# Optimization experiments

Hardware: AMD Instinct MI355X
Metric: run time of the kernel (lower is better)

The kernel has to match this reference:

```python
import jax, jax.numpy as jnp
import numpy as np

N_HEAD = 16
TEMPERATURE = 1.0
LORA_SCALING = 16.0 / 8.0  # lora_alpha / r


def setup_inputs() -> dict:
    key = jax.random.key(0)
    B, S, D, E, R = 4, 1024, 1024, 8, 8
    ks = jax.random.split(key, 24)
    it = iter(ks)

    def nrm(shape, s):
        return (jax.random.normal(next(it), shape, jnp.float32) * s)

    inp = {}
    inp['x'] = jax.random.normal(next(it), (B, S, D), jnp.float32)
    inp['conv_w'] = nrm((D, D, 3), 0.02)
    inp['conv_b'] = jnp.zeros((D,), jnp.float32)
    inp['pool_w'] = nrm((1, D), 0.02)
    inp['pool_b'] = jnp.zeros((1,), jnp.float32)
    inp['rlin_w'] = nrm((E, D), 0.02)
    inp['rlin_b'] = jnp.zeros((E,), jnp.float32)
    for p, has_bias in (('q', True), ('k', False), ('v', True), ('o', True)):
        inp[p + 'W'] = nrm((D, D), 0.02)
        if has_bias:
            inp[p + 'b'] = jnp.zeros((D,), jnp.float32)
        inp[p + 'A'] = nrm((E, R, D), 0.02)
        inp[p + 'B'] = nrm((E, D, R), 0.02)
    return inp


def _router(x, conv_w, conv_b, pool_w, pool_b, rlin_w, rlin_b):
    # Conv1d(kernel=3, padding=1) over sequence, channels = n_state
    xc = jax.lax.conv_general_dilated(
        x.transpose(0, 2, 1), conv_w, (1,), [(1, 1)],
        dimension_numbers=('NCH', 'OIH', 'NCH')) + conv_b[None, :, None]
    xp = xc.transpose(0, 2, 1)                      # [B, S, D]
    scores = xp @ pool_w.T + pool_b                 # [B, S, 1]
    w = jax.nn.softmax(scores, axis=1)
    pooled = jnp.sum(w * xp, axis=1)                # [B, D]
    logits = pooled @ rlin_w.T + rlin_b             # [B, E]
    return jax.nn.softmax(logits / TEMPERATURE, axis=-1)


def _moe_linear(x, W, b, A, Bm, route):
    base = x @ W.T
    if b is not None:
        base = base + b
    h = jnp.einsum('bsd,erd->besr', x, A)           # [B, E, S, r]
    lora = jnp.einsum('besr,enr,be->bsn', h, Bm, route)
    return base + LORA_SCALING * lora


def reference(x, conv_w, conv_b, pool_w, pool_b, rlin_w, rlin_b,
              qW, qb, qA, qB, kW, kA, kB, vW, vb, vA, vB, oW, ob, oA, oB):
    B, S, D = x.shape
    H = N_HEAD
    dh = D // H
    route = _router(x, conv_w, conv_b, pool_w, pool_b, rlin_w, rlin_b)

    q = _moe_linear(x, qW, qb, qA, qB, route)
    k = _moe_linear(x, kW, None, kA, kB, route)
    v = _moe_linear(x, vW, vb, vA, vB, route)

    scale = dh ** (-0.25)
    qh = q.reshape(B, S, H, dh).transpose(0, 2, 1, 3) * scale   # [B,H,S,dh]
    kh = k.reshape(B, S, H, dh).transpose(0, 2, 3, 1) * scale   # [B,H,dh,S]
    vh = v.reshape(B, S, H, dh).transpose(0, 2, 1, 3)           # [B,H,S,dh]

    qk = (qh @ kh).astype(jnp.float32)                          # [B,H,S,S]
    w = jax.nn.softmax(qk, axis=-1).astype(q.dtype)
    wv = (w @ vh).transpose(0, 2, 1, 3).reshape(B, S, D)

    out = _moe_linear(wv, oW, ob, oA, oB, route)
    return out, qk
```

## Files before the change

### kernel.cpp

```cpp
#include <hip/hip_runtime.h>
#include <cstdint>

typedef unsigned short u16;
typedef __bf16 bf16_t;
typedef bf16_t bf16x8 __attribute__((ext_vector_type(8)));
typedef float f32x4 __attribute__((ext_vector_type(4)));

#define B_ 4
#define S_ 1024
#define D_ 1024
#define E_ 8
#define R_ 8
#define H_ 16
#define DH_ 64

#define GLOAD16(gp, lp) __builtin_amdgcn_global_load_lds( \
        (const __attribute__((address_space(1))) void*)(gp), \
        (__attribute__((address_space(3))) void*)(lp), 16, 0, 0)

static __device__ __forceinline__ u16 f2b(float f){
    union { float f; uint32_t i; } v; v.f = f;
    uint32_t i = v.i;
    uint32_t r = i + 0x7FFFu + ((i >> 16) & 1u);
    return (u16)(r >> 16);
}

__global__ void k_pre(const float4* x, const float* qB, const float* kB,
                      const float* vB, const float* oB,
                      const float* conv_w, const float* conv_b,
                      const float* pool_w, const float* pool_b,
                      ushort4* x16, ushort4* B16v, float* cwp_part, float* constk){
    const int NCVT = 2048;
    const int NX = B_*S_*D_/4;
    const int NB = E_*D_*R_/4;
    if (blockIdx.x < NCVT){
        const int NTOT = NX + 4*NB;
        for (int i = blockIdx.x*blockDim.x + threadIdx.x; i < NTOT; i += NCVT*blockDim.x){
            if (i < NX){
                float4 v = x[i];
                ushort4 o; o.x=f2b(v.x); o.y=f2b(v.y); o.z=f2b(v.z); o.w=f2b(v.w);
                x16[i] = o;
            } else {
                int j = i - NX;
                int p = j >> 14, e = j & (NB-1);
                const float4* src = (p==0)?(const float4*)qB:(p==1)?(const float4*)kB
                                  :(p==2)?(const float4*)vB:(const float4*)oB;
                float4 v = src[e];
                ushort4 o; o.x=f2b(v.x); o.y=f2b(v.y); o.z=f2b(v.z); o.w=f2b(v.w);
                B16v[p*NB + e] = o;
            }
        }
    } else {
        int idx = blockIdx.x - NCVT;
        if (idx < 96){
            int bid = idx % 12, ob = idx / 12;
            int j = bid*256 + threadIdx.x;
            int t = j >> 10, i = j & 1023;
            float acc = 0.f;
            for (int o = ob*128; o < ob*128 + 128; ++o)
                acc += pool_w[o] * conv_w[(size_t)o*3072 + i*3 + t];
            cwp_part[ob*3072 + j] = acc;
        } else {
            __shared__ float red[256];
            float acc = 0.f;
            for (int o = threadIdx.x; o < D_; o += 256) acc += pool_w[o] * conv_b[o];
            red[threadIdx.x] = acc; __syncthreads();
            for (int s = 128; s > 0; s >>= 1){
                if (threadIdx.x < s) red[threadIdx.x] += red[threadIdx.x+s];
                __syncthreads();
            }
            if (threadIdx.x == 0) *constk = red[0] + pool_b[0];
        }
    }
}

__global__ void k_h(const float* x, const float* cwp_part, float* h){
    __shared__ float cw[3072];
    int b = blockIdx.y;
    for (int j = threadIdx.x; j < 3072; j += 256){
        float s = 0.f;
        for (int ob = 0; ob < 8; ++ob) s += cwp_part[ob*3072 + j];
        cw[j] = s;
    }
    __syncthreads();
    int w = threadIdx.x >> 6, lane = threadIdx.x & 63;
    int s = blockIdx.x*4 + w;
    const float4* xr = (const float4*)(x + ((size_t)b*S_ + s)*D_);
    const float4* c0 = (const float4*)(cw);
    const float4* c1 = (const float4*)(cw + D_);
    const float4* c2 = (const float4*)(cw + 2*D_);
    float a0 = 0.f, a1 = 0.f, a2 = 0.f;
    #pragma unroll
    for (int it = 0; it < 4; ++it){
        float4 v  = xr[it*64 + lane];
        float4 w0 = c0[it*64 + lane];
        float4 w1 = c1[it*64 + lane];
        float4 w2 = c2[it*64 + lane];
        a0 += v.x*w0.x + v.y*w0.y + v.z*w0.z + v.w*w0.w;
        a1 += v.x*w1.x + v.y*w1.y + v.z*w1.z + v.w*w1.w;
        a2 += v.x*w2.x + v.y*w2.y + v.z*w2.z + v.w*w2.w;
    }
    for (int off = 32; off; off >>= 1){
        a0 += __shfl_down(a0, off);
        a1 += __shfl_down(a1, off);
        a2 += __shfl_down(a2, off);
    }
    if (lane == 0){
        h[(0*B_ + b)*S_ + s] = a0;
        h[(1*B_ + b)*S_ + s] = a1;
        h[(2*B_ + b)*S_ + s] = a2;
    }
}

__global__ void k_xw(const float* x, const float* h, const float* constk, float* xwl){
    int b = blockIdx.y;
    int lane = threadIdx.x & 63;
    int w = threadIdx.x >> 6;
    int i = blockIdx.x*64 + lane;
    __shared__ float red[256];
    __shared__ float wsm_l[S_];
    __shared__ float red3[3][4][64];
    const float* h0 = h + (0*B_ + b)*S_;
    const float* h1 = h + (1*B_ + b)*S_;
    const float* h2 = h + (2*B_ + b)*S_;
    float ck = *constk;
    float mx = -1e30f;
    for (int s = threadIdx.x; s < S_; s += 256){
        float v = h1[s] + ck;
        if (s >= 1)   v += h0[s-1];
        if (s+1 < S_) v += h2[s+1];
        wsm_l[s] = v;
        mx = fmaxf(mx, v);
    }
    red[threadIdx.x] = mx; __syncthreads();
    for (int st = 128; st > 0; st >>= 1){
        if (threadIdx.x < st) red[threadIdx.x] = fmaxf(red[threadIdx.x], red[threadIdx.x+st]);
        __syncthreads();
    }
    mx = red[0]; __syncthreads();
    float sum = 0.f;
    for (int s = threadIdx.x; s < S_; s += 256) sum += __expf(wsm_l[s] - mx);
    red[threadIdx.x] = sum; __syncthreads();
    for (int st = 128; st > 0; st >>= 1){
        if (threadIdx.x < st) red[threadIdx.x] += red[threadIdx.x+st];
        __syncthreads();
    }
    float inv = 1.f / red[0];
    __syncthreads();
    for (int s = threadIdx.x; s < S_; s += 256)
        wsm_l[s] = __expf(wsm_l[s] - mx) * inv;
    __syncthreads();
    const float* xb = x + (size_t)b*S_*D_;
    float a0 = 0.f, a1 = 0.f, a2 = 0.f;
    #pragma unroll 4
    for (int r = w*256; r < (w+1)*256; ++r){
        float xv = xb[(size_t)r*D_ + i];
        float w1 = wsm_l[r];
        float w0 = (r+1 < S_) ? wsm_l[r+1] : 0.f;
        float w2 = (r >= 1)   ? wsm_l[r-1] : 0.f;
        a0 += w0*xv; a1 += w1*xv; a2 += w2*xv;
    }
    red3[0][w][lane] = a0; red3[1][w][lane] = a1; red3[2][w][lane] = a2;
    __syncthreads();
    if (w == 0){
        a0 = red3[0][0][lane] + red3[0][1][lane] + red3[0][2][lane] + red3[0][3][lane];
        a1 = red3[1][0][lane] + red3[1][1][lane] + red3[1][2][lane] + red3[1][3][lane];
        a2 = red3[2][0][lane] + red3[2][1][lane] + red3[2][2][lane] + red3[2][3][lane];
        xwl[b*3072 + i*3 + 0] = a0;
        xwl[b*3072 + i*3 + 1] = a1;
        xwl[b*3072 + i*3 + 2] = a2;
    }
}

__global__ void k_pooled(const float* conv_w, const float* conv_b, const float* xwl, float* pooled){
    int o = blockIdx.x*4 + (threadIdx.x >> 6);
    int lane = threadIdx.x & 63;
    const float* cw = conv_w + (size_t)o*3072;
    float a0=0.f, a1=0.f, a2=0.f, a3=0.f;
    for (int j = lane; j < 3072; j += 64){
        float c = cw[j];
        a0 += c*xwl[j]; a1 += c*xwl[3072+j]; a2 += c*xwl[2*3072+j]; a3 += c*xwl[3*3072+j];
    }
    for (int off = 32; off; off >>= 1){
        a0 += __shfl_down(a0, off); a1 += __shfl_down(a1, off);
        a2 += __shfl_down(a2, off); a3 += __shfl_down(a3, off);
    }
    if (lane == 0){
        float cb = conv_b[o];
        pooled[0*D_+o] = a0+cb; pooled[1*D_+o] = a1+cb;
        pooled[2*D_+o] = a2+cb; pooled[3*D_+o] = a3+cb;
    }
}

__global__ void k_aeff(const float* qA, const float* kA, const float* vA, const float* oA,
                       const float* pooled, const float* rlin_w, const float* rlin_b,
                       u16* AeffT){
    __shared__ float rt[E_];
    int dc = blockIdx.x, b = blockIdx.y, p = blockIdx.z;
    {
        int e = threadIdx.x >> 5, part = threadIdx.x & 31;
        float acc = 0.f;
        for (int o = part; o < D_; o += 32) acc += pooled[b*D_+o] * rlin_w[e*D_+o];
        for (int off = 16; off; off >>= 1) acc += __shfl_xor(acc, off);
        if (part == 0) rt[e] = acc + rlin_b[e];
        __syncthreads();
        if (threadIdx.x == 0){
            float mx = -1e30f;
            for (int e2 = 0; e2 < E_; ++e2) mx = fmaxf(mx, rt[e2]);
            float ex[E_], sum = 0.f;
            for (int e2 = 0; e2 < E_; ++e2){ ex[e2] = expf(rt[e2]-mx); sum += ex[e2]; }
            for (int e2 = 0; e2 < E_; ++e2) rt[e2] = ex[e2]/sum;
        }
        __syncthreads();
    }
    const float* Ap = (p==0)?qA:(p==1)?kA:(p==2)?vA:oA;
    int z = p*4 + b;
    for (int idx = threadIdx.x; idx < 64*64; idx += 256){
        int dl = idx >> 6, kk = idx & 63;
        int d = dc*64 + dl;
        int e = kk >> 3, r = kk & 7;
        float v = 2.0f * rt[e] * Ap[(size_t)(e*R_+r)*D_ + d];
        AeffT[((size_t)z*D_ + d)*64 + kk] = f2b(v);
    }
}

__global__ __launch_bounds__(256) void k_weff(
        const u16* B16,
        const float* qW, const float* kW, const float* vW, const float* oW,
        const u16* AeffT, u16* Weff){
    __shared__ __align__(16) u16 As[128*64];
    __shared__ __align__(16) u16 Bs[128*64];
    int z = blockIdx.z, p = z >> 2;
    const u16* Bp = B16 + (size_t)p*E_*D_*R_;
    const float* Wp = (p==0)?qW:(p==1)?kW:(p==2)?vW:oW;
    int n0 = blockIdx.x*128, d0 = blockIdx.y*128;
    int tid = threadIdx.x;
    int e = tid & 7, row = tid >> 3;
    for (int pass = 0; pass < 4; ++pass){
        int rr = row + pass*32;
        GLOAD16(&Bp[((size_t)e*D_ + (n0+rr))*R_],           &As[pass*2048 + tid*8]);
        GLOAD16(&AeffT[((size_t)z*D_ + (d0+rr))*64 + e*8],  &Bs[pass*2048 + tid*8]);
    }
    __syncthreads();
    int l = tid & 63, w = tid >> 6;
    int wm = (w & 1)*64, wn = (w >> 1)*64;
    int lr = l & 15, quad = l >> 4;
    f32x4 acc[4][4] = {};
    for (int kk = 0; kk < 64; kk += 32){
        bf16x8 af[4], bg[4];
        for (int i = 0; i < 4; ++i) af[i] = *(const bf16x8*)&As[(wm + i*16 + lr)*64 + kk + quad*8];
        for (int j = 0; j < 4; ++j) bg[j] = *(const bf16x8*)&Bs[(wn + j*16 + lr)*64 + kk + quad*8];
        for (int i = 0; i < 4; ++i)
            for (int j = 0; j < 4; ++j)
                acc[i][j] = __builtin_amdgcn_mfma_f32_16x16x32_bf16(af[i], bg[j], acc[i][j], 0, 0, 0);
    }
    u16* Wz = Weff + (size_t)z*D_*D_;
    for (int i = 0; i < 4; ++i)
        for (int j = 0; j < 4; ++j)
            for (int r2 = 0; r2 < 4; ++r2){
                int n = n0 + wm + i*16 + quad*4 + r2;
                int d = d0 + wn + j*16 + lr;
                Wz[(size_t)n*D_ + d] = f2b(acc[i][j][r2] + Wp[(size_t)n*D_ + d]);
            }
}

__global__ __launch_bounds__(256) void k_gemm_qkv(
        const u16* x16, const u16* Weff, u16* qkv, u16* vT, const float* qb, const float* vb){
    __shared__ __align__(16) u16 As[128*32];
    __shared__ __align__(16) u16 Bs[128*32];
    __shared__ __align__(16) u16 T[64*72];
    int z = blockIdx.z, p = z >> 2, b = z & 3;
    const u16* A  = x16 + (size_t)b*S_*D_;
    const u16* Bw = Weff + (size_t)z*D_*D_;
    int m0 = blockIdx.x*128, n0 = blockIdx.y*128;
    int tid = threadIdx.x;
    int srow = tid >> 2, skc = (tid & 3)*8;
    u16* asd = &As[tid*8];
    u16* bsd = &Bs[tid*8];
    const u16* ga0 = &A [(size_t)(m0+srow)*D_ + skc];
    const u16* ga1 = &A [(size_t)(m0+srow+64)*D_ + skc];
    const u16* gb0 = &Bw[(size_t)(n0+srow)*D_ + skc];
    const u16* gb1 = &Bw[(size_t)(n0+srow+64)*D_ + skc];
    int l = tid & 63, w = tid >> 6;
    int wm = (w & 1)*64, wn = (w >> 1)*64;
    int lr = l & 15, quad = l >> 4;
    f32x4 acc[4][4] = {};
    for (int k0 = 0; k0 < D_; k0 += 32){
        __syncthreads();
        GLOAD16(ga0 + k0, asd);
        GLOAD16(ga1 + k0, asd + 2048);
        GLOAD16(gb0 + k0, bsd);
        GLOAD16(gb1 + k0, bsd + 2048);
        __syncthreads();
        bf16x8 af[4], bg[4];
        for (int i = 0; i < 4; ++i) af[i] = *(const bf16x8*)&As[(wm + i*16 + lr)*32 + quad*8];
        for (int j = 0; j < 4; ++j) bg[j] = *(const bf16x8*)&Bs[(wn + j*16 + lr)*32 + quad*8];
        for (int i = 0; i < 4; ++i)
            for (int j = 0; j < 4; ++j)
                acc[i][j] = __builtin_amdgcn_mfma_f32_16x16x32_bf16(af[i], bg[j], acc[i][j], 0, 0, 0);
    }
    if (p < 2){
        const float* bias = (p==0) ? qb : (const float*)nullptr;
        const float scale = 0.35355339059327373f;
        u16* Cb = qkv + (size_t)z*S_*D_;
        for (int j = 0; j < 4; ++j){
            int n = n0 + wn + j*16 + lr;
            float bv = bias ? bias[n] : 0.f;
            for (int i = 0; i < 4; ++i){
                int mrow = m0 + wm + i*16 + quad*4;
                for (int r2 = 0; r2 < 4; ++r2)
                    Cb[(size_t)(mrow+r2)*D_ + n] = f2b((acc[i][j][r2] + bv)*scale);
            }
        }
    } else {
        for (int c = 0; c < 4; ++c){
            if (w == c){
                for (int j = 0; j < 4; ++j){
                    int col = j*16 + lr;
                    float bv = vb[n0 + (c>>1)*64 + col];
                    for (int i = 0; i < 4; ++i)
                        for (int r2 = 0; r2 < 4; ++r2){
                            int row = i*16 + quad*4 + r2;
                            T[row*72 + col] = f2b(acc[i][j][r2] + bv);
                        }
                }
            }
            __syncthreads();
            int bh = b*16 + (n0 >> 6) + (c >> 1);
            int s0 = m0 + (c & 1)*64;
            int dh = tid >> 2, sp = (tid & 3)*16;
            union { u16 u[8]; uint4 q; } t0_, t1_;
            for (int jj = 0; jj < 8; ++jj){
                t0_.u[jj] = T[(sp+jj)*72 + dh];
                t1_.u[jj] = T[(sp+8+jj)*72 + dh];
            }
            *(uint4*)&vT[((size_t)bh*64 + dh)*S_ + s0 + sp]     = t0_.q;
            *(uint4*)&vT[((size_t)bh*64 + dh)*S_ + s0 + sp + 8] = t1_.q;
            __syncthreads();
        }
    }
}

__global__ __launch_bounds__(256) void k_gemm_o(
        const u16* wv, const u16* WeffO, float* out, const float* ob_){
    __shared__ __align__(16) u16 As[128*32];
    __shared__ __align__(16) u16 Bs[64*32];
    int b = blockIdx.z;
    const u16* A  = wv + (size_t)b*S_*D_;
    const u16* Bw = WeffO + (size_t)b*D_*D_;
    float* Cf = out + (size_t)b*S_*D_;
    int m0 = blockIdx.x*128, n0 = blockIdx.y*64;
    int tid = threadIdx.x;
    int srow = tid >> 2, skc = (tid & 3)*8;
    u16* asd = &As[tid*8];
    u16* bsd = &Bs[tid*8];
    const u16* ga0 = &A [(size_t)(m0+srow)*D_ + skc];
    const u16* ga1 = &A [(size_t)(m0+srow+64)*D_ + skc];
    const u16* gb0 = &Bw[(size_t)(n0+srow)*D_ + skc];
    int l = tid & 63, w = tid >> 6;
    int wm = (w & 1)*64, wn = (w >> 1)*32;
    int lr = l & 15, quad = l >> 4;
    f32x4 acc[4][2] = {};
    for (int k0 = 0; k0 < D_; k0 += 32){
        __syncthreads();
        GLOAD16(ga0 + k0, asd);
        GLOAD16(ga1 + k0, asd + 2048);
        GLOAD16(gb0 + k0, bsd);
        __syncthreads();
        bf16x8 af[4], bg[2];
        for (int i = 0; i < 4; ++i) af[i] = *(const bf16x8*)&As[(wm + i*16 + lr)*32 + quad*8];
        for (int j = 0; j < 2; ++j) bg[j] = *(const bf16x8*)&Bs[(wn + j*16 + lr)*32 + quad*8];
        for (int i = 0; i < 4; ++i)
            for (int j = 0; j < 2; ++j)
                acc[i][j] = __builtin_amdgcn_mfma_f32_16x16x32_bf16(af[i], bg[j], acc[i][j], 0, 0, 0);
    }
    for (int j = 0; j < 2; ++j){
        int n = n0 + wn + j*16 + lr;
        float bv = ob_[n];
        for (int i = 0; i < 4; ++i){
            int mrow = m0 + wm + i*16 + quad*4;
            for (int r2 = 0; r2 < 4; ++r2)
                __builtin_nontemporal_store(acc[i][j][r2] + bv, &Cf[(size_t)(mrow+r2)*D_ + n]);
        }
    }
}

__global__ __launch_bounds__(256) void k_attn(const u16* q, const u16* k, const u16* vT,
                                              float* qk_out, u16* wv){
    __shared__ __align__(16) u16 Ql[64*64];
    __shared__ __align__(16) u16 Kl[64*64];
    __shared__ __align__(16) u16 Vt[64*64];
    __shared__ __align__(16) u16 Pl[64*64];
    int qt = blockIdx.x, bh = blockIdx.y;
    int b = bh >> 4, h = bh & 15;
    int q0 = qt*64;
    int tid = threadIdx.x;
    int l = tid & 63, w = tid >> 6;
    int lr = l & 15, quad = l >> 4;
    int srow = tid >> 3;
    int scol = (((tid & 7) ^ ((tid >> 3) & 7))) * 8;
    int sdst = tid * 8;
    const u16* qp  = q  + (size_t)b*S_*D_ + h*64;
    const u16* kp  = k  + (size_t)b*S_*D_ + h*64;
    const u16* vTp = vT + (size_t)bh*64*S_;
    float* qko = qk_out + (size_t)bh*S_*S_;
    GLOAD16(&qp[(size_t)(q0 + srow)*D_ + scol],      &Ql[sdst]);
    GLOAD16(&qp[(size_t)(q0 + srow + 32)*D_ + scol], &Ql[sdst + 2048]);
    int rsw = lr & 7;
    f32x4 oacc[4] = {};
    float m_i[4], l_i[4];
    for (int r2 = 0; r2 < 4; ++r2){ m_i[r2] = -1e30f; l_i[r2] = 0.f; }
    for (int t0 = 0; t0 < S_; t0 += 64){
        __syncthreads();
        GLOAD16(&kp[(size_t)(t0 + srow)*D_ + scol],        &Kl[sdst]);
        GLOAD16(&kp[(size_t)(t0 + srow + 32)*D_ + scol],   &Kl[sdst + 2048]);
        GLOAD16(&vTp[(size_t)srow*S_ + t0 + scol],         &Vt[sdst]);
        GLOAD16(&vTp[(size_t)(srow + 32)*S_ + t0 + scol],  &Vt[sdst + 2048]);
        __syncthreads();
        f32x4 sacc[4] = {};
        for (int kk = 0; kk < 64; kk += 32){
            int un = ((quad + (kk >> 3)) ^ rsw) * 8;
            bf16x8 aq = *(const bf16x8*)&Ql[(w*16 + lr)*64 + un];
            for (int jn = 0; jn < 4; ++jn){
                bf16x8 bk = *(const bf16x8*)&Kl[(jn*16 + lr)*64 + un];
                sacc[jn] = __builtin_amdgcn_mfma_f32_16x16x32_bf16(aq, bk, sacc[jn], 0, 0, 0);
            }
        }
        for (int jn = 0; jn < 4; ++jn)
            for (int r2 = 0; r2 < 4; ++r2){
                int sq = q0 + w*16 + quad*4 + r2;
                __builtin_nontemporal_store(sacc[jn][r2], &qko[(size_t)sq*S_ + t0 + jn*16 + lr]);
            }
        float alpha[4];
        for (int r2 = 0; r2 < 4; ++r2){
            float mx = fmaxf(fmaxf(sacc[0][r2], sacc[1][r2]), fmaxf(sacc[2][r2], sacc[3][r2]));
            for (int off = 1; off < 16; off <<= 1) mx = fmaxf(mx, __shfl_xor(mx, off));
            float mnew = fmaxf(m_i[r2], mx);
            alpha[r2] = __expf(m_i[r2] - mnew);
            m_i[r2] = mnew;
        }
        f32x4 p[4];
        for (int jn = 0; jn < 4; ++jn)
            for (int r2 = 0; r2 < 4; ++r2)
                p[jn][r2] = __expf(sacc[jn][r2] - m_i[r2]);
        for (int r2 = 0; r2 < 4; ++r2){
            float s = p[0][r2] + p[1][r2] + p[2][r2] + p[3][r2];
            for (int off = 1; off < 16; off <<= 1) s += __shfl_xor(s, off);
            l_i[r2] = l_i[r2]*alpha[r2] + s;
        }
        for (int jn = 0; jn < 4; ++jn)
            for (int r2 = 0; r2 < 4; ++r2)
                oacc[jn][r2] *= alpha[r2];
        for (int jn = 0; jn < 4; ++jn)
            for (int r2 = 0; r2 < 4; ++r2){
                int pr = w*16 + quad*4 + r2;
                int tu = (jn*2 + (lr >> 3)) ^ (pr & 7);
                Pl[pr*64 + tu*8 + (lr & 7)] = f2b(p[jn][r2]);
            }
        for (int kk = 0; kk < 64; kk += 32){
            int un = ((quad + (kk >> 3)) ^ rsw) * 8;
            bf16x8 ap = *(const bf16x8*)&Pl[(w*16 + lr)*64 + un];
            for (int jn = 0; jn < 4; ++jn){
                bf16x8 bv = *(const bf16x8*)&Vt[(jn*16 + lr)*64 + un];
                oacc[jn] = __builtin_amdgcn_mfma_f32_16x16x32_bf16(ap, bv, oacc[jn], 0, 0, 0);
            }
        }
    }
    u16* wvp = wv + (size_t)b*S_*D_ + h*64;
    for (int r2 = 0; r2 < 4; ++r2){
        float inv = 1.f / l_i[r2];
        int sq = q0 + w*16 + quad*4 + r2;
        for (int jn = 0; jn < 4; ++jn)
            wvp[(size_t)sq*D_ + jn*16 + lr] = f2b(oacc[jn][r2] * inv);
    }
}

extern "C" void kernel_launch(void* const* d_in, const int* in_sizes, int n_in,
                              void* d_out, int out_size, void* d_ws, size_t ws_size,
                              hipStream_t stream){
    const float* x      = (const float*)d_in[0];
    const float* conv_w = (const float*)d_in[1];
    const float* conv_b = (const float*)d_in[2];
    const float* pool_w = (const float*)d_in[3];
    const float* pool_b = (const float*)d_in[4];
    const float* rlin_w = (const float*)d_in[5];
    const float* rlin_b = (const float*)d_in[6];
    const float* qW = (const float*)d_in[7];
    const float* qb = (const float*)d_in[8];
    const float* qA = (const float*)d_in[9];
    const float* qB = (const float*)d_in[10];
    const float* kW = (const float*)d_in[11];
    const float* kA = (const float*)d_in[12];
    const float* kB = (const float*)d_in[13];
    const float* vW = (const float*)d_in[14];
    const float* vb = (const float*)d_in[15];
    const float* vA = (const float*)d_in[16];
    const float* vB = (const float*)d_in[17];
    const float* oW = (const float*)d_in[18];
    const float* ob = (const float*)d_in[19];
    const float* oA = (const float*)d_in[20];
    const float* oB = (const float*)d_in[21];

    char* ws = (char*)d_ws;
    float* constk   = (float*)(ws + 512);
    float* cwp_part = (float*)(ws + 1024);
    float* h        = (float*)(ws + 131072);
    float* xwl      = (float*)(ws + 196608);
    float* pooled   = (float*)(ws + 262144);
    u16* AeffT = (u16*)(ws + (1ull  << 20));
    u16* B16   = (u16*)(ws + (3ull  << 20));
    u16* Weff  = (u16*)(ws + (4ull  << 20));
    u16* x16   = (u16*)(ws + (36ull << 20));
    u16* qkv   = (u16*)(ws + (44ull << 20));
    u16* qbuf  = qkv + 0*(size_t)B_*S_*D_;
    u16* kbuf  = qkv + 1*(size_t)B_*S_*D_;
    u16* vbuf  = qkv + 2*(size_t)B_*S_*D_;
    u16* vTbuf = (u16*)(ws + (68ull << 20));
    u16* wvbuf = vbuf;

    float* out    = (float*)d_out;
    float* qk_out = out + (size_t)B_*S_*D_;

    const long long sDD = (long long)D_*D_;

    k_pre<<<2145, 256, 0, stream>>>((const float4*)x, qB, kB, vB, oB,
                                    conv_w, conv_b, pool_w, pool_b,
                                    (ushort4*)x16, (ushort4*)B16, cwp_part, constk);
    k_h     <<<dim3(S_/4, B_), 256, 0, stream>>>(x, cwp_part, h);
    k_xw    <<<dim3(16, B_), 256, 0, stream>>>(x, h, constk, xwl);
    k_pooled<<<256, 256, 0, stream>>>(conv_w, conv_b, xwl, pooled);
    k_aeff  <<<dim3(16, B_, 4), 256, 0, stream>>>(qA, kA, vA, oA, pooled, rlin_w, rlin_b, AeffT);
    k_weff  <<<dim3(8, 8, 16), 256, 0, stream>>>(B16, qW, kW, vW, oW, AeffT, Weff);
    k_gemm_qkv<<<dim3(8,8,12), 256, 0, stream>>>(x16, Weff, qkv, vTbuf, qb, vb);
    k_attn  <<<dim3(16, B_*H_), 256, 0, stream>>>(qbuf, kbuf, vTbuf, qk_out, wvbuf);
    k_gemm_o<<<dim3(8,16,B_), 256, 0, stream>>>(wvbuf, Weff + 12*sDD, out, ob);
}
```

Before: 580.0 us.

## Double-buffer LDS tiles in QKV, output GEMMs and attention kernel

Adds double-buffered shared-memory tiles to the QKV GEMM, the output GEMM and the attention kernel. The next K-slice or KV-tile is prefetched via global_load_lds while the current one is consumed by MFMA, and the two barriers per iteration become one. The aim is to hide global load latency behind compute. In exchange LDS use doubles, which may lower occupancy. The loads into LDS need vmcnt waits before the barrier, so the overlap depends on how the compiler places those waits.

```diff
diff --git a/kernel.cpp b/kernel.cpp
--- a/kernel.cpp
+++ b/kernel.cpp
@@ -266,8 +266,8 @@
 
 __global__ __launch_bounds__(256) void k_gemm_qkv(
         const u16* x16, const u16* Weff, u16* qkv, u16* vT, const float* qb, const float* vb){
-    __shared__ __align__(16) u16 As[128*32];
-    __shared__ __align__(16) u16 Bs[128*32];
+    __shared__ __align__(16) u16 As[2][128*32];
+    __shared__ __align__(16) u16 Bs[2][128*32];
     __shared__ __align__(16) u16 T[64*72];
     int z = blockIdx.z, p = z >> 2, b = z & 3;
     const u16* A  = x16 + (size_t)b*S_*D_;
@@ -275,8 +275,6 @@
     int m0 = blockIdx.x*128, n0 = blockIdx.y*128;
     int tid = threadIdx.x;
     int srow = tid >> 2, skc = (tid & 3)*8;
-    u16* asd = &As[tid*8];
-    u16* bsd = &Bs[tid*8];
     const u16* ga0 = &A [(size_t)(m0+srow)*D_ + skc];
     const u16* ga1 = &A [(size_t)(m0+srow+64)*D_ + skc];
     const u16* gb0 = &Bw[(size_t)(n0+srow)*D_ + skc];
@@ -285,19 +283,28 @@
     int wm = (w & 1)*64, wn = (w >> 1)*64;
     int lr = l & 15, quad = l >> 4;
     f32x4 acc[4][4] = {};
+    GLOAD16(ga0, &As[0][tid*8]);
+    GLOAD16(ga1, &As[0][tid*8 + 2048]);
+    GLOAD16(gb0, &Bs[0][tid*8]);
+    GLOAD16(gb1, &Bs[0][tid*8 + 2048]);
+    __syncthreads();
+    int cur = 0;
     for (int k0 = 0; k0 < D_; k0 += 32){
-        __syncthreads();
-        GLOAD16(ga0 + k0, asd);
-        GLOAD16(ga1 + k0, asd + 2048);
-        GLOAD16(gb0 + k0, bsd);
-        GLOAD16(gb1 + k0, bsd + 2048);
-        __syncthreads();
+        int nk = k0 + 32;
+        if (nk < D_){
+            GLOAD16(ga0 + nk, &As[cur^1][tid*8]);
+            GLOAD16(ga1 + nk, &As[cur^1][tid*8 + 2048]);
+            GLOAD16(gb0 + nk, &Bs[cur^1][tid*8]);
+            GLOAD16(gb1 + nk, &Bs[cur^1][tid*8 + 2048]);
+        }
         bf16x8 af[4], bg[4];
-        for (int i = 0; i < 4; ++i) af[i] = *(const bf16x8*)&As[(wm + i*16 + lr)*32 + quad*8];
-        for (int j = 0; j < 4; ++j) bg[j] = *(const bf16x8*)&Bs[(wn + j*16 + lr)*32 + quad*8];
+        for (int i = 0; i < 4; ++i) af[i] = *(const bf16x8*)&As[cur][(wm + i*16 + lr)*32 + quad*8];
+        for (int j = 0; j < 4; ++j) bg[j] = *(const bf16x8*)&Bs[cur][(wn + j*16 + lr)*32 + quad*8];
         for (int i = 0; i < 4; ++i)
             for (int j = 0; j < 4; ++j)
                 acc[i][j] = __builtin_amdgcn_mfma_f32_16x16x32_bf16(af[i], bg[j], acc[i][j], 0, 0, 0);
+        __syncthreads();
+        cur ^= 1;
     }
     if (p < 2){
         const float* bias = (p==0) ? qb : (const float*)nullptr;
@@ -343,8 +350,8 @@
 
 __global__ __launch_bounds__(256) void k_gemm_o(
         const u16* wv, const u16* WeffO, float* out, const float* ob_){
-    __shared__ __align__(16) u16 As[128*32];
-    __shared__ __align__(16) u16 Bs[64*32];
+    __shared__ __align__(16) u16 As[2][128*32];
+    __shared__ __align__(16) u16 Bs[2][64*32];
     int b = blockIdx.z;
     const u16* A  = wv + (size_t)b*S_*D_;
     const u16* Bw = WeffO + (size_t)b*D_*D_;
@@ -352,8 +359,6 @@
     int m0 = blockIdx.x*128, n0 = blockIdx.y*64;
     int tid = threadIdx.x;
     int srow = tid >> 2, skc = (tid & 3)*8;
-    u16* asd = &As[tid*8];
-    u16* bsd = &Bs[tid*8];
     const u16* ga0 = &A [(size_t)(m0+srow)*D_ + skc];
     const u16* ga1 = &A [(size_t)(m0+srow+64)*D_ + skc];
     const u16* gb0 = &Bw[(size_t)(n0+srow)*D_ + skc];
@@ -361,18 +366,26 @@
     int wm = (w & 1)*64, wn = (w >> 1)*32;
     int lr = l & 15, quad = l >> 4;
     f32x4 acc[4][2] = {};
+    GLOAD16(ga0, &As[0][tid*8]);
+    GLOAD16(ga1, &As[0][tid*8 + 2048]);
+    GLOAD16(gb0, &Bs[0][tid*8]);
+    __syncthreads();
+    int cur = 0;
     for (int k0 = 0; k0 < D_; k0 += 32){
-        __syncthreads();
-        GLOAD16(ga0 + k0, asd);
-        GLOAD16(ga1 + k0, asd + 2048);
-        GLOAD16(gb0 + k0, bsd);
-        __syncthreads();
+        int nk = k0 + 32;
+        if (nk < D_){
+            GLOAD16(ga0 + nk, &As[cur^1][tid*8]);
+            GLOAD16(ga1 + nk, &As[cur^1][tid*8 + 2048]);
+            GLOAD16(gb0 + nk, &Bs[cur^1][tid*8]);
+        }
         bf16x8 af[4], bg[2];
-        for (int i = 0; i < 4; ++i) af[i] = *(const bf16x8*)&As[(wm + i*16 + lr)*32 + quad*8];
-        for (int j = 0; j < 2; ++j) bg[j] = *(const bf16x8*)&Bs[(wn + j*16 + lr)*32 + quad*8];
+        for (int i = 0; i < 4; ++i) af[i] = *(const bf16x8*)&As[cur][(wm + i*16 + lr)*32 + quad*8];
+        for (int j = 0; j < 2; ++j) bg[j] = *(const bf16x8*)&Bs[cur][(wn + j*16 + lr)*32 + quad*8];
         for (int i = 0; i < 4; ++i)
             for (int j = 0; j < 2; ++j)
                 acc[i][j] = __builtin_amdgcn_mfma_f32_16x16x32_bf16(af[i], bg[j], acc[i][j], 0, 0, 0);
+        __syncthreads();
+        cur ^= 1;
     }
     for (int j = 0; j < 2; ++j){
         int n = n0 + wn + j*16 + lr;
@@ -388,8 +401,8 @@
 __global__ __launch_bounds__(256) void k_attn(const u16* q, const u16* k, const u16* vT,
                                               float* qk_out, u16* wv){
     __shared__ __align__(16) u16 Ql[64*64];
-    __shared__ __align__(16) u16 Kl[64*64];
-    __shared__ __align__(16) u16 Vt[64*64];
+    __shared__ __align__(16) u16 Kl[2][64*64];
+    __shared__ __align__(16) u16 Vt[2][64*64];
     __shared__ __align__(16) u16 Pl[64*64];
     int qt = blockIdx.x, bh = blockIdx.y;
     int b = bh >> 4, h = bh & 15;
@@ -406,23 +419,30 @@
     float* qko = qk_out + (size_t)bh*S_*S_;
     GLOAD16(&qp[(size_t)(q0 + srow)*D_ + scol],      &Ql[sdst]);
     GLOAD16(&qp[(size_t)(q0 + srow + 32)*D_ + scol], &Ql[sdst + 2048]);
+    GLOAD16(&kp[(size_t)srow*D_ + scol],             &Kl[0][sdst]);
+    GLOAD16(&kp[(size_t)(srow + 32)*D_ + scol],      &Kl[0][sdst + 2048]);
+    GLOAD16(&vTp[(size_t)srow*S_ + scol],            &Vt[0][sdst]);
+    GLOAD16(&vTp[(size_t)(srow + 32)*S_ + scol],     &Vt[0][sdst + 2048]);
+    __syncthreads();
     int rsw = lr & 7;
+    int cur = 0;
     f32x4 oacc[4] = {};
     float m_i[4], l_i[4];
     for (int r2 = 0; r2 < 4; ++r2){ m_i[r2] = -1e30f; l_i[r2] = 0.f; }
     for (int t0 = 0; t0 < S_; t0 += 64){
-        __syncthreads();
-        GLOAD16(&kp[(size_t)(t0 + srow)*D_ + scol],        &Kl[sdst]);
-        GLOAD16(&kp[(size_t)(t0 + srow + 32)*D_ + scol],   &Kl[sdst + 2048]);
-        GLOAD16(&vTp[(size_t)srow*S_ + t0 + scol],         &Vt[sdst]);
-        GLOAD16(&vTp[(size_t)(srow + 32)*S_ + t0 + scol],  &Vt[sdst + 2048]);
-        __syncthreads();
+        int t1 = t0 + 64;
+        if (t1 < S_){
+            GLOAD16(&kp[(size_t)(t1 + srow)*D_ + scol],        &Kl[cur^1][sdst]);
+            GLOAD16(&kp[(size_t)(t1 + srow + 32)*D_ + scol],   &Kl[cur^1][sdst + 2048]);
+            GLOAD16(&vTp[(size_t)srow*S_ + t1 + scol],         &Vt[cur^1][sdst]);
+            GLOAD16(&vTp[(size_t)(srow + 32)*S_ + t1 + scol],  &Vt[cur^1][sdst + 2048]);
+        }
         f32x4 sacc[4] = {};
         for (int kk = 0; kk < 64; kk += 32){
             int un = ((quad + (kk >> 3)) ^ rsw) * 8;
             bf16x8 aq = *(const bf16x8*)&Ql[(w*16 + lr)*64 + un];
             for (int jn = 0; jn < 4; ++jn){
-                bf16x8 bk = *(const bf16x8*)&Kl[(jn*16 + lr)*64 + un];
+                bf16x8 bk = *(const bf16x8*)&Kl[cur][(jn*16 + lr)*64 + un];
                 sacc[jn] = __builtin_amdgcn_mfma_f32_16x16x32_bf16(aq, bk, sacc[jn], 0, 0, 0);
             }
         }
@@ -461,10 +481,12 @@
             int un = ((quad + (kk >> 3)) ^ rsw) * 8;
             bf16x8 ap = *(const bf16x8*)&Pl[(w*16 + lr)*64 + un];
             for (int jn = 0; jn < 4; ++jn){
-                bf16x8 bv = *(const bf16x8*)&Vt[(jn*16 + lr)*64 + un];
+                bf16x8 bv = *(const bf16x8*)&Vt[cur][(jn*16 + lr)*64 + un];
                 oacc[jn] = __builtin_amdgcn_mfma_f32_16x16x32_bf16(ap, bv, oacc[jn], 0, 0, 0);
             }
         }
+        __syncthreads();
+        cur ^= 1;
     }
     u16* wvp = wv + (size_t)b*S_*D_ + h*64;
     for (int r2 = 0; r2 < 4; ++r2){
```

New measurement: 618.0 us. 6.5% more time.
